# Performance work log

Measured on AMD Instinct MI355X. Metric: run time of the kernel, lower is better.

The kernel has to match this reference:

```python
import jax, jax.numpy as jnp
import numpy as np

D = 128          # fine voxel grid resolution
N0 = 250000
D_IN, D_BASE, D_OUT = 16, 8, 8
EPS = 1e-5
# (cin, cout) for conv0..conv6, conv7, conv9, conv11
_CH = [(16, 8), (8, 16), (16, 16), (16, 32), (32, 32), (32, 64), (64, 64), (64, 32), (32, 16), (16, 8)]

def _offsets():
    r = np.arange(-1, 2)
    return np.stack(np.meshgrid(r, r, r, indexing='ij'), -1).reshape(-1, 3)  # [27,3]

def _lookup_fn(coords, d):
    keys = (coords[:, 0].astype(np.int64) * d + coords[:, 1]) * d + coords[:, 2]
    order = np.argsort(keys)
    skeys = keys[order]
    def lookup(q):
        valid = ((q >= 0) & (q < d)).all(-1)
        k = (q[:, 0].astype(np.int64) * d + q[:, 1]) * d + q[:, 2]
        pos = np.clip(np.searchsorted(skeys, k), 0, len(skeys) - 1)
        return np.where(valid & (skeys[pos] == k), order[pos], -1).astype(np.int32)
    return lookup

def _nbr_same(coords, d):
    # stride-1 sparse conv: outputs at input coords, neighbors at coord+k
    lk = _lookup_fn(coords, d)
    return np.stack([lk(coords + o) for o in _offsets()], 1)  # [N,27]

def _nbr_down(c_out, c_in, d_in):
    # stride-2 conv: output p gathers inputs at 2p+k
    lk = _lookup_fn(c_in, d_in)
    return np.stack([lk(c_out * 2 + o) for o in _offsets()], 1)

def _nbr_up(c_out, c_in, d_in):
    # transposed stride-2 conv: output q gathers input p=(q-k)/2 where divisible
    lk = _lookup_fn(c_in, d_in)
    cols = []
    for o in _offsets():
        q = c_out - o
        div = (q % 2 == 0).all(-1)
        cols.append(np.where(div, lk(q // 2), -1).astype(np.int32))
    return np.stack(cols, 1)

def setup_inputs():
    rng = np.random.default_rng(0)
    flat = rng.choice(D ** 3, size=N0, replace=False)
    c0 = np.stack([flat // (D * D), (flat // D) % D, flat % D], 1).astype(np.int32)
    c1 = np.unique(c0 // 2, axis=0)
    c2 = np.unique(c1 // 2, axis=0)
    c3 = np.unique(c2 // 2, axis=0)
    inp = {
        'feats': jax.random.normal(jax.random.key(0), (N0, D_IN), jnp.float32),
        'nbr0': jnp.asarray(_nbr_same(c0, D)),
        'nbr_d01': jnp.asarray(_nbr_down(c1, c0, D)),
        'nbr1': jnp.asarray(_nbr_same(c1, D // 2)),
        'nbr_d12': jnp.asarray(_nbr_down(c2, c1, D // 2)),
        'nbr2': jnp.asarray(_nbr_same(c2, D // 4)),
        'nbr_d23': jnp.asarray(_nbr_down(c3, c2, D // 4)),
        'nbr3': jnp.asarray(_nbr_same(c3, D // 8)),
        'nbr_u32': jnp.asarray(_nbr_up(c2, c3, D // 8)),
        'nbr_u21': jnp.asarray(_nbr_up(c1, c2, D // 4)),
        'nbr_u10': jnp.asarray(_nbr_up(c0, c1, D // 2)),
    }
    key = jax.random.key(1)
    for i, (ci, co) in enumerate(_CH):
        key, kw = jax.random.split(key)
        inp['w%d' % i] = jax.random.normal(kw, (27, ci, co), jnp.float32) / np.sqrt(27.0 * ci)
        inp['g%d' % i] = jnp.ones((co,), jnp.float32)
        inp['b%d' % i] = jnp.zeros((co,), jnp.float32)
    inp['lin_w'] = jax.random.normal(jax.random.key(2), (D_OUT, D_BASE), jnp.float32) / np.sqrt(D_BASE)
    return inp

def _sconv_bn_relu(f, nbr, w, g, b):
    # f: [Nin,Cin], nbr: [Nout,27] (-1 = no neighbor), w: [27,Cin,Cout]
    gth = jnp.where((nbr >= 0)[..., None], f[jnp.maximum(nbr, 0)], 0.0)  # [Nout,27,Cin]
    y = jnp.einsum('nkc,kco->no', gth, w)
    mu = y.mean(0)                       # training-mode BatchNorm over active voxels
    var = y.var(0)
    return jax.nn.relu((y - mu) * jax.lax.rsqrt(var + EPS) * g + b)

def reference(feats, nbr0, nbr_d01, nbr1, nbr_d12, nbr2, nbr_d23, nbr3, nbr_u32, nbr_u21, nbr_u10,
              w0, g0, b0, w1, g1, b1, w2, g2, b2, w3, g3, b3, w4, g4, b4,
              w5, g5, b5, w6, g6, b6, w7, g7, b7, w8, g8, b8, w9, g9, b9, lin_w):
    c0f = _sconv_bn_relu(feats, nbr0, w0, g0, b0)
    c2f = _sconv_bn_relu(_sconv_bn_relu(c0f, nbr_d01, w1, g1, b1), nbr1, w2, g2, b2)
    c4f = _sconv_bn_relu(_sconv_bn_relu(c2f, nbr_d12, w3, g3, b3), nbr2, w4, g4, b4)
    x = _sconv_bn_relu(_sconv_bn_relu(c4f, nbr_d23, w5, g5, b5), nbr3, w6, g6, b6)
    x = c4f + _sconv_bn_relu(x, nbr_u32, w7, g7, b7)
    x = c2f + _sconv_bn_relu(x, nbr_u21, w8, g8, b8)
    x = c0f + _sconv_bn_relu(x, nbr_u10, w9, g9, b9)
    return x @ lin_w.T, x
```

## Files before the change

### kernel.cpp

```cpp
#include <hip/hip_runtime.h>

#define EPSV 1e-5f

typedef __attribute__((ext_vector_type(8))) short short8;
typedef __attribute__((ext_vector_type(4))) float float4v;

static inline int cdiv(int a, int b) { return (a + b - 1) / b; }
static inline int imin(int a, int b) { return a < b ? a : b; }

__device__ inline unsigned short f2bf(float x) {
  unsigned u = __float_as_uint(x);
  return (unsigned short)((u + 0x7FFFu + ((u >> 16) & 1u)) >> 16);
}
__device__ inline float bf2f(unsigned short u) {
  return __uint_as_float(((unsigned)u) << 16);
}

#define NBUCKET 64

struct PrepArgs {
  const float* w[10];
  unsigned short* wt[10];
  int ci[10];
  int co[10];
  int wcum[11];
  const float* feats;
  unsigned short* featsb;
  int nfeat4;
  float* stats;
};

__global__ __launch_bounds__(256) void prep_kernel(PrepArgs p, long total) {
  const int nstat4 = 10 * NBUCKET * 128 / 4;
  for (long tid0 = (long)blockIdx.x * 256 + threadIdx.x; tid0 < total;
       tid0 += (long)gridDim.x * 256) {
    long tid = tid0;
    if (tid < nstat4) {
      ((float4*)p.stats)[tid] = make_float4(0.f, 0.f, 0.f, 0.f);
      continue;
    }
    tid -= nstat4;
    if (tid < p.nfeat4) {
      float4 v = ((const float4*)p.feats)[tid];
      ushort4 r;
      r.x = f2bf(v.x); r.y = f2bf(v.y); r.z = f2bf(v.z); r.w = f2bf(v.w);
      ((ushort4*)p.featsb)[tid] = r;
      continue;
    }
    tid -= p.nfeat4;
    if (tid >= p.wcum[10]) continue;
    int i = 0;
    while (tid >= p.wcum[i + 1]) ++i;
    int e = (int)(tid - p.wcum[i]);
    int ci = p.ci[i], co = p.co[i];
    int k = e / (ci * co);
    int r = e - k * (ci * co);
    int o = r / ci;
    int c = r - o * ci;
    float val = p.w[i][((long)k * ci + c) * co + o];
    if (ci >= 32) {
      int chunk, quad, j;
      if (ci == 32) { chunk = k; quad = c >> 3; j = c & 7; }
      else { chunk = k * 2 + (c >> 5); int rem = c & 31; quad = rem >> 3; j = rem & 7; }
      int lane_ = quad * 16 + (o & 15);
      int cb = o >> 4;
      long dst = (((long)chunk * (co >> 4) + cb) * 64 + lane_) * 8 + j;
      p.wt[i][dst] = f2bf(val);
    } else {
      p.wt[i][((long)k * co + o) * ci + c] = f2bf(val);
    }
  }
}

template<int CI, int CO>
__global__ __launch_bounds__(256) void conv_mfma(
    const unsigned short* __restrict__ f, const int* __restrict__ nbr,
    const unsigned short* __restrict__ wtd, unsigned short* __restrict__ y,
    float* __restrict__ stats, int nout, int ntiles) {
  constexpr int NCHUNK = (CI == 8) ? 7 : (CI == 16) ? 14 : (CI == 32) ? 27 : 54;
  __shared__ int sIdx[4 * 448];

  const int tid = threadIdx.x;
  const int lane = tid & 63;
  const int wid = tid >> 6;
  const int m = lane & 15;
  const int quad = lane >> 4;
  const int cbase = blockIdx.y * 16;
  const int co = cbase + m;
  const bool cok = co < CO;
  int* myIdx = &sIdx[wid * 448];

  auto tapof = [&](int c) -> int {
    if constexpr (CI == 8) return c * 4 + quad;
    else if constexpr (CI == 16) return c * 2 + (quad >> 1);
    else if constexpr (CI == 32) return c;
    else return c >> 1;
  };
  auto cioof = [&](int c) -> int {
    if constexpr (CI == 8) return 0;
    else if constexpr (CI == 16) return (quad & 1) * 8;
    else if constexpr (CI == 32) return quad * 8;
    else return ((c & 1) << 5) + quad * 8;
  };

  float sum = 0.f, sq = 0.f;

  if constexpr (CI <= 16) {
    short8 Bv[NCHUNK];
#pragma unroll
    for (int c = 0; c < NCHUNK; ++c) {
      int tap = tapof(c);
      short8 bq;
#pragma unroll
      for (int q = 0; q < 8; ++q) bq[q] = 0;
      if (cok && tap < 27)
        bq = *(const short8*)(wtd + ((long)tap * CO + co) * CI + cioof(c));
      Bv[c] = bq;
    }
    for (int tile = blockIdx.x; tile < ntiles; tile += gridDim.x) {
      const int rowb = tile * 64 + wid * 16;
      {
        const int* src = nbr + (long)rowb * 27;
#pragma unroll
        for (int j = 0; j < 7; ++j) {
          int off = j * 64 + lane;
          int v = -1;
          if (off < 432) {
            int r = off / 27;
            if (rowb + r < nout) v = src[off];
          }
          myIdx[off] = v;
        }
      }
      unsigned actm = 0;
      int idxs[NCHUNK];
#pragma unroll
      for (int c = 0; c < NCHUNK; ++c) {
        int tap = tapof(c);
        int idx = (tap < 27) ? myIdx[m * 27 + tap] : -1;
        idxs[c] = idx;
        if (__ballot(idx >= 0) != 0ull) actm |= 1u << c;
      }
      short8 A[NCHUNK];
#pragma unroll
      for (int c = 0; c < NCHUNK; ++c) {
        short8 a;
#pragma unroll
        for (int q = 0; q < 8; ++q) a[q] = 0;
        if ((actm >> c) & 1) {
          if (idxs[c] >= 0) a = *(const short8*)(f + (long)idxs[c] * CI + cioof(c));
        }
        A[c] = a;
      }
      float4v acc = {0.f, 0.f, 0.f, 0.f};
#pragma unroll
      for (int c = 0; c < NCHUNK; ++c)
        if ((actm >> c) & 1)
          acc = __builtin_amdgcn_mfma_f32_16x16x32_bf16(A[c], Bv[c], acc, 0, 0, 0);
#pragma unroll
      for (int r = 0; r < 4; ++r) {
        float v = acc[r];
        int orow = tile * 64 + wid * 16 + quad * 4 + r;
        if (cok && orow < nout) y[(long)orow * CO + co] = f2bf(v);
        sum += v;
        sq = fmaf(v, v, sq);
      }
    }
  } else {
    constexpr int G = 9;
    constexpr int NG = NCHUNK / G;
    for (int tile = blockIdx.x; tile < ntiles; tile += gridDim.x) {
      const int rowb = tile * 64 + wid * 16;
      {
        const int* src = nbr + (long)rowb * 27;
#pragma unroll
        for (int j = 0; j < 7; ++j) {
          int off = j * 64 + lane;
          int v = -1;
          if (off < 432) {
            int r = off / 27;
            if (rowb + r < nout) v = src[off];
          }
          myIdx[off] = v;
        }
      }
      unsigned long long actm = 0;
#pragma unroll
      for (int c = 0; c < NCHUNK; ++c) {
        int idx = myIdx[m * 27 + tapof(c)];
        if (__ballot(idx >= 0) != 0ull) actm |= 1ull << c;
      }
      short8 A[2][G], B[2][G];
      auto load_group = [&](int g, int bi) {
#pragma unroll
        for (int j2 = 0; j2 < G; ++j2) {
          const int c = g * G + j2;
          short8 a, bq;
#pragma unroll
          for (int q = 0; q < 8; ++q) { a[q] = 0; bq[q] = 0; }
          if ((actm >> c) & 1) {
            int idx = myIdx[m * 27 + tapof(c)];
            if (idx >= 0) a = *(const short8*)(f + (long)idx * CI + cioof(c));
            bq = *(const short8*)(wtd + (((long)c * (CO / 16) + blockIdx.y) * 64 + lane) * 8);
          }
          A[bi][j2] = a; B[bi][j2] = bq;
        }
      };
      float4v acc = {0.f, 0.f, 0.f, 0.f};
      load_group(0, 0);
#pragma unroll
      for (int g = 0; g < NG; ++g) {
        const int cur = g & 1;
        if (g + 1 < NG) load_group(g + 1, cur ^ 1);
#pragma unroll
        for (int j2 = 0; j2 < G; ++j2)
          if ((actm >> (g * G + j2)) & 1)
            acc = __builtin_amdgcn_mfma_f32_16x16x32_bf16(A[cur][j2], B[cur][j2], acc, 0, 0, 0);
      }
#pragma unroll
      for (int r = 0; r < 4; ++r) {
        float v = acc[r];
        int orow = tile * 64 + wid * 16 + quad * 4 + r;
        if (orow < nout) y[(long)orow * CO + co] = f2bf(v);
        sum += v;
        sq = fmaf(v, v, sq);
      }
    }
  }

  sum += __shfl_xor(sum, 16); sq += __shfl_xor(sq, 16);
  sum += __shfl_xor(sum, 32); sq += __shfl_xor(sq, 32);
  if (quad == 0 && cok) {
    float* st = stats + ((((unsigned)blockIdx.x * 4 + wid) & (NBUCKET - 1)) << 7);
    atomicAdd(&st[co], sum);
    atomicAdd(&st[64 + co], sq);
  }
}

template<int CO>
__global__ __launch_bounds__(256) void bn_relu_bf16(
    const unsigned short* __restrict__ y, const float* __restrict__ stats,
    const float* __restrict__ g, const float* __restrict__ b,
    const unsigned short* __restrict__ skip, unsigned short* __restrict__ out,
    int nout, float inv_n) {
  __shared__ float sA[CO], sC[CO];
  if ((int)threadIdx.x < CO) {
    int o = threadIdx.x;
    float su = 0.f, sq = 0.f;
#pragma unroll 8
    for (int bk = 0; bk < NBUCKET; ++bk) {
      su += stats[bk * 128 + o];
      sq += stats[bk * 128 + 64 + o];
    }
    float mu = su * inv_n;
    float var = sq * inv_n - mu * mu;
    float a = g[o] * rsqrtf(var + EPSV);
    sA[o] = a;
    sC[o] = fmaf(-mu, a, b[o]);
  }
  __syncthreads();
  long total4 = (long)nout * CO / 4;
  for (long i4 = (long)blockIdx.x * 256 + threadIdx.x; i4 < total4;
       i4 += (long)gridDim.x * 256) {
    int o = (int)((i4 * 4) % CO);
    ushort4 v = ((const ushort4*)y)[i4];
    float vv[4] = {bf2f(v.x), bf2f(v.y), bf2f(v.z), bf2f(v.w)};
    unsigned short rr[4];
#pragma unroll
    for (int j = 0; j < 4; ++j) {
      float x = fmaxf(fmaf(vv[j], sA[o + j], sC[o + j]), 0.f);
      if (skip) x += bf2f(skip[i4 * 4 + j]);
      rr[j] = f2bf(x);
    }
    ushort4 r;
    r.x = rr[0]; r.y = rr[1]; r.z = rr[2]; r.w = rr[3];
    ((ushort4*)out)[i4] = r;
  }
}

__global__ __launch_bounds__(256) void tail_kernel(
    const unsigned short* __restrict__ c0f, const float* __restrict__ st9,
    const float* __restrict__ g9, const float* __restrict__ b9, float inv_n,
    const float* __restrict__ lin_w, const unsigned short* __restrict__ y9,
    float* __restrict__ out0, float* __restrict__ x0, int n0) {
  __shared__ float swl[64];
  __shared__ float sbn[16];
  if (threadIdx.x < 64) swl[threadIdx.x] = lin_w[threadIdx.x];
  if (threadIdx.x < 8) {
    int o = threadIdx.x;
    float su = 0.f, sq = 0.f;
#pragma unroll 8
    for (int bk = 0; bk < NBUCKET; ++bk) {
      su += st9[bk * 128 + o];
      sq += st9[bk * 128 + 64 + o];
    }
    float mu = su * inv_n;
    float var = sq * inv_n - mu * mu;
    float a = g9[o] * rsqrtf(var + EPSV);
    sbn[o] = a;
    sbn[8 + o] = fmaf(-mu, a, b9[o]);
  }
  __syncthreads();
  for (int n = blockIdx.x * 256 + threadIdx.x; n < n0; n += gridDim.x * 256) {
    const ushort4* pr = (const ushort4*)(y9 + (long)n * 8);
    ushort4 r0 = pr[0], r1 = pr[1];
    unsigned short rw[8] = {r0.x, r0.y, r0.z, r0.w, r1.x, r1.y, r1.z, r1.w};
    const ushort4* pc = (const ushort4*)(c0f + (long)n * 8);
    ushort4 c0 = pc[0], c1 = pc[1];
    unsigned short cs[8] = {c0.x, c0.y, c0.z, c0.w, c1.x, c1.y, c1.z, c1.w};
    float xv[8];
#pragma unroll
    for (int c = 0; c < 8; ++c)
      xv[c] = bf2f(cs[c]) + fmaxf(fmaf(bf2f(rw[c]), sbn[c], sbn[8 + c]), 0.f);
    *(float4*)(x0 + (long)n * 8) = make_float4(xv[0], xv[1], xv[2], xv[3]);
    *(float4*)(x0 + (long)n * 8 + 4) = make_float4(xv[4], xv[5], xv[6], xv[7]);
    float ov[8];
#pragma unroll
    for (int j = 0; j < 8; ++j) {
      float s = 0.f;
#pragma unroll
      for (int c = 0; c < 8; ++c) s = fmaf(xv[c], swl[j * 8 + c], s);
      ov[j] = s;
    }
    *(float4*)(out0 + (long)n * 8) = make_float4(ov[0], ov[1], ov[2], ov[3]);
    *(float4*)(out0 + (long)n * 8 + 4) = make_float4(ov[4], ov[5], ov[6], ov[7]);
  }
}

extern "C" void kernel_launch(void* const* d_in, const int* in_sizes, int n_in,
                              void* d_out, int out_size, void* d_ws, size_t ws_size,
                              hipStream_t stream) {
  const float* feats   = (const float*)d_in[0];
  const int* nbr0      = (const int*)d_in[1];
  const int* nbr_d01   = (const int*)d_in[2];
  const int* nbr1      = (const int*)d_in[3];
  const int* nbr_d12   = (const int*)d_in[4];
  const int* nbr2      = (const int*)d_in[5];
  const int* nbr_d23   = (const int*)d_in[6];
  const int* nbr3      = (const int*)d_in[7];
  const int* nbr_u32   = (const int*)d_in[8];
  const int* nbr_u21   = (const int*)d_in[9];
  const int* nbr_u10   = (const int*)d_in[10];
  const float* w[10];
  const float* g[10];
  const float* b[10];
  for (int i = 0; i < 10; ++i) {
    w[i] = (const float*)d_in[11 + 3 * i];
    g[i] = (const float*)d_in[12 + 3 * i];
    b[i] = (const float*)d_in[13 + 3 * i];
  }
  const float* lin_w = (const float*)d_in[41];

  const int N0 = in_sizes[0] / 16;
  const int N1 = in_sizes[2] / 27;
  const int N2 = in_sizes[4] / 27;
  const int N3 = in_sizes[6] / 27;
  const float i0 = 1.f / N0, i1 = 1.f / N1, i2 = 1.f / N2, i3 = 1.f / N3;

  static const int CIv[10] = {16, 8, 16, 16, 32, 32, 64, 64, 32, 16};
  static const int COv[10] = {8, 16, 16, 32, 32, 64, 64, 32, 16, 8};

  float* stats = (float*)d_ws;
  unsigned short* u = (unsigned short*)(stats + 10 * NBUCKET * 128);

  unsigned short* yraw = u; u += (size_t)N1 * 32;

  unsigned short* wt[10];
  int wcum[11];
  wcum[0] = 0;
  for (int i = 0; i < 10; ++i) {
    wt[i] = u;
    int sz = 27 * CIv[i] * COv[i];
    u += sz;
    wcum[i + 1] = wcum[i] + sz;
  }
  unsigned short* featsb = u; u += (size_t)N0 * 16;
  unsigned short* c0f = u;    u += (size_t)N0 * 8;
  unsigned short* t1  = u;    u += (size_t)N1 * 16;
  unsigned short* c2f = u;    u += (size_t)N1 * 16;
  unsigned short* t2  = u;    u += (size_t)N2 * 32;
  unsigned short* c4f = u;    u += (size_t)N2 * 32;
  unsigned short* t3  = u;    u += (size_t)N3 * 64;
  unsigned short* t4  = u;    u += (size_t)N3 * 64;
  unsigned short* t5  = t2;
  unsigned short* t6  = t1;
  float* out0 = (float*)d_out;
  float* x0   = (float*)d_out + (size_t)N0 * 8;

  float* s[10];
  for (int i = 0; i < 10; ++i) s[i] = stats + i * NBUCKET * 128;

  PrepArgs pa;
  for (int i = 0; i < 10; ++i) {
    pa.w[i] = w[i]; pa.wt[i] = wt[i];
    pa.ci[i] = CIv[i]; pa.co[i] = COv[i];
    pa.wcum[i] = wcum[i];
  }
  pa.wcum[10] = wcum[10];
  pa.feats = feats; pa.featsb = featsb;
  pa.nfeat4 = N0 * 16 / 4;
  pa.stats = stats;
  long prep_total = (10 * NBUCKET * 128 / 4) + pa.nfeat4 + wcum[10];
  prep_kernel<<<imin((int)((prep_total + 255) / 256), 2048), 256, 0, stream>>>(pa, prep_total);

  auto bgrid = [](long nout, int co) {
    return imin((int)((nout * co / 4 + 255) / 256), 1024);
  };
  auto cgrid = [](int ntiles) { return imin(ntiles, 1024); };

  int tb0 = cdiv(N0, 64), tb1 = cdiv(N1, 64), tb2 = cdiv(N2, 64), tb3 = cdiv(N3, 64);

  conv_mfma<16, 8><<<dim3(cgrid(tb0), 1), 256, 0, stream>>>(featsb, nbr0, wt[0], yraw, s[0], N0, tb0);
  bn_relu_bf16<8><<<bgrid(N0, 8), 256, 0, stream>>>(yraw, s[0], g[0], b[0], nullptr, c0f, N0, i0);

  conv_mfma<8, 16><<<dim3(cgrid(tb1), 1), 256, 0, stream>>>(c0f, nbr_d01, wt[1], yraw, s[1], N1, tb1);
  bn_relu_bf16<16><<<bgrid(N1, 16), 256, 0, stream>>>(yraw, s[1], g[1], b[1], nullptr, t1, N1, i1);

  conv_mfma<16, 16><<<dim3(cgrid(tb1), 1), 256, 0, stream>>>(t1, nbr1, wt[2], yraw, s[2], N1, tb1);
  bn_relu_bf16<16><<<bgrid(N1, 16), 256, 0, stream>>>(yraw, s[2], g[2], b[2], nullptr, c2f, N1, i1);

  conv_mfma<16, 32><<<dim3(cgrid(tb2), 2), 256, 0, stream>>>(c2f, nbr_d12, wt[3], yraw, s[3], N2, tb2);
  bn_relu_bf16<32><<<bgrid(N2, 32), 256, 0, stream>>>(yraw, s[3], g[3], b[3], nullptr, t2, N2, i2);

  conv_mfma<32, 32><<<dim3(cgrid(tb2), 2), 256, 0, stream>>>(t2, nbr2, wt[4], yraw, s[4], N2, tb2);
  bn_relu_bf16<32><<<bgrid(N2, 32), 256, 0, stream>>>(yraw, s[4], g[4], b[4], nullptr, c4f, N2, i2);

  conv_mfma<32, 64><<<dim3(cgrid(tb3), 4), 256, 0, stream>>>(c4f, nbr_d23, wt[5], yraw, s[5], N3, tb3);
  bn_relu_bf16<64><<<bgrid(N3, 64), 256, 0, stream>>>(yraw, s[5], g[5], b[5], nullptr, t3, N3, i3);

  conv_mfma<64, 64><<<dim3(cgrid(tb3), 4), 256, 0, stream>>>(t3, nbr3, wt[6], yraw, s[6], N3, tb3);
  bn_relu_bf16<64><<<bgrid(N3, 64), 256, 0, stream>>>(yraw, s[6], g[6], b[6], nullptr, t4, N3, i3);

  conv_mfma<64, 32><<<dim3(cgrid(tb2), 2), 256, 0, stream>>>(t4, nbr_u32, wt[7], yraw, s[7], N2, tb2);
  bn_relu_bf16<32><<<bgrid(N2, 32), 256, 0, stream>>>(yraw, s[7], g[7], b[7], c4f, t5, N2, i2);

  conv_mfma<32, 16><<<dim3(cgrid(tb1), 1), 256, 0, stream>>>(t5, nbr_u21, wt[8], yraw, s[8], N1, tb1);
  bn_relu_bf16<16><<<bgrid(N1, 16), 256, 0, stream>>>(yraw, s[8], g[8], b[8], c2f, t6, N1, i1);

  conv_mfma<16, 8><<<dim3(cgrid(tb0), 1), 256, 0, stream>>>(t6, nbr_u10, wt[9], yraw, s[9], N0, tb0);

  tail_kernel<<<imin(cdiv(N0, 256), 1024), 256, 0, stream>>>(
      c0f, s[9], g[9], b[9], i0, lin_w, yraw, out0, x0, N0);
}
```

Before: 520.8 us.

## Fuse BN+ReLU of previous layer into conv gather, drop standalone BN kernels

Each conv now reads the previous layer's raw pre-BN outputs and applies BatchNorm and ReLU on the fly as neighbor features are gathered. This removes seven standalone bn_relu passes and their launches. Skip connections are handled by a combine kernel that normalizes both branches. The shared-memory staging of neighbor indices is replaced with direct per-lane global loads of nbr. In exchange, the per-element BN transform is recomputed for every gathered tap (up to 27 times per voxel), the index loads are uncoalesced, and more intermediate buffers are kept alive.

```diff
diff --git a/kernel.cpp b/kernel.cpp
--- a/kernel.cpp
+++ b/kernel.cpp
@@ -72,13 +72,16 @@
   }
 }
 
-template<int CI, int CO>
+template<int CI, int CO, int FUSE>
 __global__ __launch_bounds__(256) void conv_mfma(
-    const unsigned short* __restrict__ f, const int* __restrict__ nbr,
-    const unsigned short* __restrict__ wtd, unsigned short* __restrict__ y,
-    float* __restrict__ stats, int nout, int ntiles) {
+    const unsigned short* __restrict__ f,
+    const float* __restrict__ fstats, const float* __restrict__ fg,
+    const float* __restrict__ fb, float finv,
+    const int* __restrict__ nbr, const unsigned short* __restrict__ wtd,
+    unsigned short* __restrict__ y, float* __restrict__ stats,
+    int nout, int ntiles) {
   constexpr int NCHUNK = (CI == 8) ? 7 : (CI == 16) ? 14 : (CI == 32) ? 27 : 54;
-  __shared__ int sIdx[4 * 448];
+  __shared__ float sBN[FUSE ? 2 * CI : 2];
 
   const int tid = threadIdx.x;
   const int lane = tid & 63;
@@ -88,7 +91,41 @@
   const int cbase = blockIdx.y * 16;
   const int co = cbase + m;
   const bool cok = co < CO;
-  int* myIdx = &sIdx[wid * 448];
+
+  if constexpr (FUSE) {
+    if (tid < CI) {
+      float su = 0.f, sqv = 0.f;
+#pragma unroll 8
+      for (int bk = 0; bk < NBUCKET; ++bk) {
+        su += fstats[bk * 128 + tid];
+        sqv += fstats[bk * 128 + 64 + tid];
+      }
+      float mu = su * finv;
+      float var = sqv * finv - mu * mu;
+      float a = fg[tid] * rsqrtf(var + EPSV);
+      sBN[tid] = a;
+      sBN[CI + tid] = fmaf(-mu, a, fb[tid]);
+    }
+    __syncthreads();
+  }
+
+  float wA0[8], wC0[8], wA1[8], wC1[8];
+  if constexpr (FUSE) {
+    int base0 = (CI == 8) ? 0 : (CI == 16) ? (quad & 1) * 8 : quad * 8;
+#pragma unroll
+    for (int j = 0; j < 8; ++j) {
+      wA0[j] = sBN[base0 + j];
+      wC0[j] = sBN[CI + base0 + j];
+    }
+    if constexpr (CI == 64) {
+      int base1 = 32 + quad * 8;
+#pragma unroll
+      for (int j = 0; j < 8; ++j) {
+        wA1[j] = sBN[base1 + j];
+        wC1[j] = sBN[CI + base1 + j];
+      }
+    }
+  }
 
   auto tapof = [&](int c) -> int {
     if constexpr (CI == 8) return c * 4 + quad;
@@ -102,6 +139,21 @@
     else if constexpr (CI == 32) return quad * 8;
     else return ((c & 1) << 5) + quad * 8;
   };
+  auto xform = [&](short8 raw, int c) -> short8 {
+    if constexpr (!FUSE) return raw;
+    const float* A = wA0; const float* C = wC0;
+    if constexpr (CI == 64) {
+      if (c & 1) { A = wA1; C = wC1; }
+    }
+    short8 r;
+#pragma unroll
+    for (int j = 0; j < 8; ++j) {
+      float v = bf2f((unsigned short)raw[j]);
+      v = fmaxf(fmaf(v, A[j], C[j]), 0.f);
+      r[j] = (short)f2bf(v);
+    }
+    return r;
+  };
 
   float sum = 0.f, sq = 0.f;
 
@@ -119,25 +171,14 @@
     }
     for (int tile = blockIdx.x; tile < ntiles; tile += gridDim.x) {
       const int rowb = tile * 64 + wid * 16;
-      {
-        const int* src = nbr + (long)rowb * 27;
-#pragma unroll
-        for (int j = 0; j < 7; ++j) {
-          int off = j * 64 + lane;
-          int v = -1;
-          if (off < 432) {
-            int r = off / 27;
-            if (rowb + r < nout) v = src[off];
-          }
-          myIdx[off] = v;
-        }
-      }
+      const int row = rowb + m;
+      const bool rok = row < nout;
       unsigned actm = 0;
       int idxs[NCHUNK];
 #pragma unroll
       for (int c = 0; c < NCHUNK; ++c) {
         int tap = tapof(c);
-        int idx = (tap < 27) ? myIdx[m * 27 + tap] : -1;
+        int idx = (rok && tap < 27) ? nbr[(long)row * 27 + tap] : -1;
         idxs[c] = idx;
         if (__ballot(idx >= 0) != 0ull) actm |= 1u << c;
       }
@@ -148,7 +189,10 @@
 #pragma unroll
         for (int q = 0; q < 8; ++q) a[q] = 0;
         if ((actm >> c) & 1) {
-          if (idxs[c] >= 0) a = *(const short8*)(f + (long)idxs[c] * CI + cioof(c));
+          if (idxs[c] >= 0) {
+            a = *(const short8*)(f + (long)idxs[c] * CI + cioof(c));
+            a = xform(a, c);
+          }
         }
         A[c] = a;
       }
@@ -160,7 +204,7 @@
 #pragma unroll
       for (int r = 0; r < 4; ++r) {
         float v = acc[r];
-        int orow = tile * 64 + wid * 16 + quad * 4 + r;
+        int orow = rowb + quad * 4 + r;
         if (cok && orow < nout) y[(long)orow * CO + co] = f2bf(v);
         sum += v;
         sq = fmaf(v, v, sq);
@@ -171,25 +215,18 @@
     constexpr int NG = NCHUNK / G;
     for (int tile = blockIdx.x; tile < ntiles; tile += gridDim.x) {
       const int rowb = tile * 64 + wid * 16;
-      {
-        const int* src = nbr + (long)rowb * 27;
-#pragma unroll
-        for (int j = 0; j < 7; ++j) {
-          int off = j * 64 + lane;
-          int v = -1;
-          if (off < 432) {
-            int r = off / 27;
-            if (rowb + r < nout) v = src[off];
-          }
-          myIdx[off] = v;
-        }
-      }
+      const int row = rowb + m;
+      const bool rok = row < nout;
+      int idxs[27];
       unsigned long long actm = 0;
 #pragma unroll
-      for (int c = 0; c < NCHUNK; ++c) {
-        int idx = myIdx[m * 27 + tapof(c)];
-        if (__ballot(idx >= 0) != 0ull) actm |= 1ull << c;
-      }
+      for (int t = 0; t < 27; ++t) {
+        idxs[t] = rok ? nbr[(long)row * 27 + t] : -1;
+      }
+#pragma unroll
+      for (int c = 0; c < NCHUNK; ++c)
+        if (__ballot(idxs[tapof(c)] >= 0) != 0ull) actm |= 1ull << c;
+
       short8 A[2][G], B[2][G];
       auto load_group = [&](int g, int bi) {
 #pragma unroll
@@ -199,8 +236,11 @@
 #pragma unroll
           for (int q = 0; q < 8; ++q) { a[q] = 0; bq[q] = 0; }
           if ((actm >> c) & 1) {
-            int idx = myIdx[m * 27 + tapof(c)];
-            if (idx >= 0) a = *(const short8*)(f + (long)idx * CI + cioof(c));
+            int idx = idxs[tapof(c)];
+            if (idx >= 0) {
+              a = *(const short8*)(f + (long)idx * CI + cioof(c));
+              a = xform(a, c);
+            }
             bq = *(const short8*)(wtd + (((long)c * (CO / 16) + blockIdx.y) * 64 + lane) * 8);
           }
           A[bi][j2] = a; B[bi][j2] = bq;
@@ -220,7 +260,7 @@
 #pragma unroll
       for (int r = 0; r < 4; ++r) {
         float v = acc[r];
-        int orow = tile * 64 + wid * 16 + quad * 4 + r;
+        int orow = rowb + quad * 4 + r;
         if (orow < nout) y[(long)orow * CO + co] = f2bf(v);
         sum += v;
         sq = fmaf(v, v, sq);
@@ -238,38 +278,42 @@
 }
 
 template<int CO>
-__global__ __launch_bounds__(256) void bn_relu_bf16(
-    const unsigned short* __restrict__ y, const float* __restrict__ stats,
-    const float* __restrict__ g, const float* __restrict__ b,
-    const unsigned short* __restrict__ skip, unsigned short* __restrict__ out,
-    int nout, float inv_n) {
-  __shared__ float sA[CO], sC[CO];
+__global__ __launch_bounds__(256) void bn2_combine(
+    const unsigned short* __restrict__ ya, const float* __restrict__ sa,
+    const float* __restrict__ ga, const float* __restrict__ ba,
+    const unsigned short* __restrict__ yb, const float* __restrict__ sb,
+    const float* __restrict__ gb, const float* __restrict__ bb,
+    float inv_n, unsigned short* __restrict__ out, int nout) {
+  __shared__ float cA[CO], cC[CO], cA2[CO], cC2[CO];
   if ((int)threadIdx.x < CO) {
     int o = threadIdx.x;
-    float su = 0.f, sq = 0.f;
+    float su = 0.f, sqv = 0.f, su2 = 0.f, sq2 = 0.f;
 #pragma unroll 8
     for (int bk = 0; bk < NBUCKET; ++bk) {
-      su += stats[bk * 128 + o];
-      sq += stats[bk * 128 + 64 + o];
-    }
-    float mu = su * inv_n;
-    float var = sq * inv_n - mu * mu;
-    float a = g[o] * rsqrtf(var + EPSV);
-    sA[o] = a;
-    sC[o] = fmaf(-mu, a, b[o]);
+      su += sa[bk * 128 + o];  sqv += sa[bk * 128 + 64 + o];
+      su2 += sb[bk * 128 + o]; sq2 += sb[bk * 128 + 64 + o];
+    }
+    float mu = su * inv_n, var = sqv * inv_n - mu * mu;
+    float a = ga[o] * rsqrtf(var + EPSV);
+    cA[o] = a; cC[o] = fmaf(-mu, a, ba[o]);
+    float mu2 = su2 * inv_n, var2 = sq2 * inv_n - mu2 * mu2;
+    float a2 = gb[o] * rsqrtf(var2 + EPSV);
+    cA2[o] = a2; cC2[o] = fmaf(-mu2, a2, bb[o]);
   }
   __syncthreads();
   long total4 = (long)nout * CO / 4;
   for (long i4 = (long)blockIdx.x * 256 + threadIdx.x; i4 < total4;
        i4 += (long)gridDim.x * 256) {
     int o = (int)((i4 * 4) % CO);
-    ushort4 v = ((const ushort4*)y)[i4];
-    float vv[4] = {bf2f(v.x), bf2f(v.y), bf2f(v.z), bf2f(v.w)};
+    ushort4 va = ((const ushort4*)ya)[i4];
+    ushort4 vb = ((const ushort4*)yb)[i4];
+    unsigned short aw[4] = {va.x, va.y, va.z, va.w};
+    unsigned short bw[4] = {vb.x, vb.y, vb.z, vb.w};
     unsigned short rr[4];
 #pragma unroll
     for (int j = 0; j < 4; ++j) {
-      float x = fmaxf(fmaf(vv[j], sA[o + j], sC[o + j]), 0.f);
-      if (skip) x += bf2f(skip[i4 * 4 + j]);
+      float x = fmaxf(fmaf(bf2f(aw[j]), cA[o + j], cC[o + j]), 0.f) +
+                fmaxf(fmaf(bf2f(bw[j]), cA2[o + j], cC2[o + j]), 0.f);
       rr[j] = f2bf(x);
     }
     ushort4 r;
@@ -279,39 +323,43 @@
 }
 
 __global__ __launch_bounds__(256) void tail_kernel(
-    const unsigned short* __restrict__ c0f, const float* __restrict__ st9,
+    const unsigned short* __restrict__ y0, const float* __restrict__ s0,
+    const float* __restrict__ g0, const float* __restrict__ b0,
+    const unsigned short* __restrict__ y9, const float* __restrict__ s9,
     const float* __restrict__ g9, const float* __restrict__ b9, float inv_n,
-    const float* __restrict__ lin_w, const unsigned short* __restrict__ y9,
+    const float* __restrict__ lin_w,
     float* __restrict__ out0, float* __restrict__ x0, int n0) {
   __shared__ float swl[64];
-  __shared__ float sbn[16];
+  __shared__ float sbn[32];
   if (threadIdx.x < 64) swl[threadIdx.x] = lin_w[threadIdx.x];
   if (threadIdx.x < 8) {
     int o = threadIdx.x;
-    float su = 0.f, sq = 0.f;
+    float su = 0.f, sqv = 0.f, su2 = 0.f, sq2 = 0.f;
 #pragma unroll 8
     for (int bk = 0; bk < NBUCKET; ++bk) {
-      su += st9[bk * 128 + o];
-      sq += st9[bk * 128 + 64 + o];
-    }
-    float mu = su * inv_n;
-    float var = sq * inv_n - mu * mu;
-    float a = g9[o] * rsqrtf(var + EPSV);
-    sbn[o] = a;
-    sbn[8 + o] = fmaf(-mu, a, b9[o]);
+      su += s0[bk * 128 + o];  sqv += s0[bk * 128 + 64 + o];
+      su2 += s9[bk * 128 + o]; sq2 += s9[bk * 128 + 64 + o];
+    }
+    float mu = su * inv_n, var = sqv * inv_n - mu * mu;
+    float a = g0[o] * rsqrtf(var + EPSV);
+    sbn[o] = a; sbn[8 + o] = fmaf(-mu, a, b0[o]);
+    float mu2 = su2 * inv_n, var2 = sq2 * inv_n - mu2 * mu2;
+    float a2 = g9[o] * rsqrtf(var2 + EPSV);
+    sbn[16 + o] = a2; sbn[24 + o] = fmaf(-mu2, a2, b9[o]);
   }
   __syncthreads();
   for (int n = blockIdx.x * 256 + threadIdx.x; n < n0; n += gridDim.x * 256) {
-    const ushort4* pr = (const ushort4*)(y9 + (long)n * 8);
-    ushort4 r0 = pr[0], r1 = pr[1];
-    unsigned short rw[8] = {r0.x, r0.y, r0.z, r0.w, r1.x, r1.y, r1.z, r1.w};
-    const ushort4* pc = (const ushort4*)(c0f + (long)n * 8);
-    ushort4 c0 = pc[0], c1 = pc[1];
-    unsigned short cs[8] = {c0.x, c0.y, c0.z, c0.w, c1.x, c1.y, c1.z, c1.w};
+    const ushort4* p0 = (const ushort4*)(y0 + (long)n * 8);
+    ushort4 a0 = p0[0], a1 = p0[1];
+    unsigned short aw[8] = {a0.x, a0.y, a0.z, a0.w, a1.x, a1.y, a1.z, a1.w};
+    const ushort4* p9 = (const ushort4*)(y9 + (long)n * 8);
+    ushort4 c0 = p9[0], c1 = p9[1];
+    unsigned short cw[8] = {c0.x, c0.y, c0.z, c0.w, c1.x, c1.y, c1.z, c1.w};
     float xv[8];
 #pragma unroll
     for (int c = 0; c < 8; ++c)
-      xv[c] = bf2f(cs[c]) + fmaxf(fmaf(bf2f(rw[c]), sbn[c], sbn[8 + c]), 0.f);
+      xv[c] = fmaxf(fmaf(bf2f(aw[c]), sbn[c], sbn[8 + c]), 0.f) +
+              fmaxf(fmaf(bf2f(cw[c]), sbn[16 + c], sbn[24 + c]), 0.f);
     *(float4*)(x0 + (long)n * 8) = make_float4(xv[0], xv[1], xv[2], xv[3]);
     *(float4*)(x0 + (long)n * 8 + 4) = make_float4(xv[4], xv[5], xv[6], xv[7]);
     float ov[8];
@@ -363,8 +411,6 @@
   float* stats = (float*)d_ws;
   unsigned short* u = (unsigned short*)(stats + 10 * NBUCKET * 128);
 
-  unsigned short* yraw = u; u += (size_t)N1 * 32;
-
   unsigned short* wt[10];
   int wcum[11];
   wcum[0] = 0;
@@ -375,15 +421,18 @@
     wcum[i + 1] = wcum[i] + sz;
   }
   unsigned short* featsb = u; u += (size_t)N0 * 16;
-  unsigned short* c0f = u;    u += (size_t)N0 * 8;
-  unsigned short* t1  = u;    u += (size_t)N1 * 16;
-  unsigned short* c2f = u;    u += (size_t)N1 * 16;
-  unsigned short* t2  = u;    u += (size_t)N2 * 32;
-  unsigned short* c4f = u;    u += (size_t)N2 * 32;
-  unsigned short* t3  = u;    u += (size_t)N3 * 64;
-  unsigned short* t4  = u;    u += (size_t)N3 * 64;
-  unsigned short* t5  = t2;
-  unsigned short* t6  = t1;
+  unsigned short* y0 = u;  u += (size_t)N0 * 8;
+  unsigned short* y1 = u;  u += (size_t)N1 * 16;
+  unsigned short* y2 = u;  u += (size_t)N1 * 16;
+  unsigned short* y3 = u;  u += (size_t)N2 * 32;
+  unsigned short* y4 = u;  u += (size_t)N2 * 32;
+  unsigned short* y5 = u;  u += (size_t)N3 * 64;
+  unsigned short* y6 = u;  u += (size_t)N3 * 64;
+  unsigned short* y7 = u;  u += (size_t)N2 * 32;
+  unsigned short* y8 = u;  u += (size_t)N1 * 16;
+  unsigned short* y9 = u;  u += (size_t)N0 * 8;
+  unsigned short* x2 = u;  u += (size_t)N2 * 32;
+  unsigned short* x1 = u;  u += (size_t)N1 * 16;
   float* out0 = (float*)d_out;
   float* x0   = (float*)d_out + (size_t)N0 * 8;
 
@@ -403,42 +452,49 @@
   long prep_total = (10 * NBUCKET * 128 / 4) + pa.nfeat4 + wcum[10];
   prep_kernel<<<imin((int)((prep_total + 255) / 256), 2048), 256, 0, stream>>>(pa, prep_total);
 
-  auto bgrid = [](long nout, int co) {
+  auto cgrid = [](int ntiles) { return imin(ntiles, 1024); };
+  auto b2grid = [](long nout, int co) {
     return imin((int)((nout * co / 4 + 255) / 256), 1024);
   };
-  auto cgrid = [](int ntiles) { return imin(ntiles, 1024); };
 
   int tb0 = cdiv(N0, 64), tb1 = cdiv(N1, 64), tb2 = cdiv(N2, 64), tb3 = cdiv(N3, 64);
 
-  conv_mfma<16, 8><<<dim3(cgrid(tb0), 1), 256, 0, stream>>>(featsb, nbr0, wt[0], yraw, s[0], N0, tb0);
-  bn_relu_bf16<8><<<bgrid(N0, 8), 256, 0, stream>>>(yraw, s[0], g[0], b[0], nullptr, c0f, N0, i0);
-
-  conv_mfma<8, 16><<<dim3(cgrid(tb1), 1), 256, 0, stream>>>(c0f, nbr_d01, wt[1], yraw, s[1], N1, tb1);
-  bn_relu_bf16<16><<<bgrid(N1, 16), 256, 0, stream>>>(yraw, s[1], g[1], b[1], nullptr, t1, N1, i1);
-
-  conv_mfma<16, 16><<<dim3(cgrid(tb1), 1), 256, 0, stream>>>(t1, nbr1, wt[2], yraw, s[2], N1, tb1);
-  bn_relu_bf16<16><<<bgrid(N1, 16), 256, 0, stream>>>(yraw, s[2], g[2], b[2], nullptr, c2f, N1, i1);
-
-  conv_mfma<16, 32><<<dim3(cgrid(tb2), 2), 256, 0, stream>>>(c2f, nbr_d12, wt[3], yraw, s[3], N2, tb2);
-  bn_relu_bf16<32><<<bgrid(N2, 32), 256, 0, stream>>>(yraw, s[3], g[3], b[3], nullptr, t2, N2, i2);
-
-  conv_mfma<32, 32><<<dim3(cgrid(tb2), 2), 256, 0, stream>>>(t2, nbr2, wt[4], yraw, s[4], N2, tb2);
-  bn_relu_bf16<32><<<bgrid(N2, 32), 256, 0, stream>>>(yraw, s[4], g[4], b[4], nullptr, c4f, N2, i2);
-
-  conv_mfma<32, 64><<<dim3(cgrid(tb3), 4), 256, 0, stream>>>(c4f, nbr_d23, wt[5], yraw, s[5], N3, tb3);
-  bn_relu_bf16<64><<<bgrid(N3, 64), 256, 0, stream>>>(yraw, s[5], g[5], b[5], nullptr, t3, N3, i3);
-
-  conv_mfma<64, 64><<<dim3(cgrid(tb3), 4), 256, 0, stream>>>(t3, nbr3, wt[6], yraw, s[6], N3, tb3);
-  bn_relu_bf16<64><<<bgrid(N3, 64), 256, 0, stream>>>(yraw, s[6], g[6], b[6], nullptr, t4, N3, i3);
-
-  conv_mfma<64, 32><<<dim3(cgrid(tb2), 2), 256, 0, stream>>>(t4, nbr_u32, wt[7], yraw, s[7], N2, tb2);
-  bn_relu_bf16<32><<<bgrid(N2, 32), 256, 0, stream>>>(yraw, s[7], g[7], b[7], c4f, t5, N2, i2);
-
-  conv_mfma<32, 16><<<dim3(cgrid(tb1), 1), 256, 0, stream>>>(t5, nbr_u21, wt[8], yraw, s[8], N1, tb1);
-  bn_relu_bf16<16><<<bgrid(N1, 16), 256, 0, stream>>>(yraw, s[8], g[8], b[8], c2f, t6, N1, i1);
-
-  conv_mfma<16, 8><<<dim3(cgrid(tb0), 1), 256, 0, stream>>>(t6, nbr_u10, wt[9], yraw, s[9], N0, tb0);
+  conv_mfma<16, 8, 0><<<dim3(cgrid(tb0), 1), 256, 0, stream>>>(
+      featsb, nullptr, nullptr, nullptr, 0.f, nbr0, wt[0], y0, s[0], N0, tb0);
+
+  conv_mfma<8, 16, 1><<<dim3(cgrid(tb1), 1), 256, 0, stream>>>(
+      y0, s[0], g[0], b[0], i0, nbr_d01, wt[1], y1, s[1], N1, tb1);
+
+  conv_mfma<16, 16, 1><<<dim3(cgrid(tb1), 1), 256, 0, stream>>>(
+      y1, s[1], g[1], b[1], i1, nbr1, wt[2], y2, s[2], N1, tb1);
+
+  conv_mfma<16, 32, 1><<<dim3(cgrid(tb2), 2), 256, 0, stream>>>(
+      y2, s[2], g[2], b[2], i1, nbr_d12, wt[3], y3, s[3], N2, tb2);
+
+  conv_mfma<32, 32, 1><<<dim3(cgrid(tb2), 2), 256, 0, stream>>>(
+      y3, s[3], g[3], b[3], i2, nbr2, wt[4], y4, s[4], N2, tb2);
+
+  conv_mfma<32, 64, 1><<<dim3(cgrid(tb3), 4), 256, 0, stream>>>(
+      y4, s[4], g[4], b[4], i2, nbr_d23, wt[5], y5, s[5], N3, tb3);
+
+  conv_mfma<64, 64, 1><<<dim3(cgrid(tb3), 4), 256, 0, stream>>>(
+      y5, s[5], g[5], b[5], i3, nbr3, wt[6], y6, s[6], N3, tb3);
+
+  conv_mfma<64, 32, 1><<<dim3(cgrid(tb2), 2), 256, 0, stream>>>(
+      y6, s[6], g[6], b[6], i3, nbr_u32, wt[7], y7, s[7], N2, tb2);
+
+  bn2_combine<32><<<b2grid(N2, 32), 256, 0, stream>>>(
+      y4, s[4], g[4], b[4], y7, s[7], g[7], b[7], i2, x2, N2);
+
+  conv_mfma<32, 16, 0><<<dim3(cgrid(tb1), 1), 256, 0, stream>>>(
+      x2, nullptr, nullptr, nullptr, 0.f, nbr_u21, wt[8], y8, s[8], N1, tb1);
+
+  bn2_combine<16><<<b2grid(N1, 16), 256, 0, stream>>>(
+      y2, s[2], g[2], b[2], y8, s[8], g[8], b[8], i1, x1, N1);
+
+  conv_mfma<16, 8, 0><<<dim3(cgrid(tb0), 1), 256, 0, stream>>>(
+      x1, nullptr, nullptr, nullptr, 0.f, nbr_u10, wt[9], y9, s[9], N0, tb0);
 
   tail_kernel<<<imin(cdiv(N0, 256), 1024), 256, 0, stream>>>(
-      c0f, s[9], g[9], b[9], i0, lin_w, yraw, out0, x0, N0);
-}
+      y0, s[0], g[0], b[0], y9, s[9], g[9], b[9], i0, lin_w, out0, x0, N0);
+}
```

New measurement: 593.0 us. 1.14x slower.
